# Performance work log

Hardware: AMD Instinct MI355X
Metric: run time of the kernel (lower is better)

Reference implementation:

```python
import jax, jax.numpy as jnp
import numpy as np

N_EMBED = 64
HEAD_SIZE = 64
B, T = 4096, 128

def setup_inputs() -> dict:
    key = jax.random.key(0)
    k0, k1, k2, k3 = jax.random.split(key, 4)
    x = jax.random.normal(k0, (B, T, N_EMBED), dtype=jnp.float32)
    # nn.Linear(N_EMBED, head_size, bias=False): weight shape [head_size, N_EMBED], y = x @ W.T
    Wq = jax.random.normal(k1, (HEAD_SIZE, N_EMBED), dtype=jnp.float32) * (1.0 / np.sqrt(N_EMBED))
    Wk = jax.random.normal(k2, (HEAD_SIZE, N_EMBED), dtype=jnp.float32) * (1.0 / np.sqrt(N_EMBED))
    Wv = jax.random.normal(k3, (HEAD_SIZE, N_EMBED), dtype=jnp.float32) * (1.0 / np.sqrt(N_EMBED))
    return {"x": x, "Wq": Wq, "Wk": Wk, "Wv": Wv}

def reference(x, Wq, Wk, Wv):
    # q,k,v: [B,T,H]
    q = jnp.einsum('btc,hc->bth', x, Wq)
    k = jnp.einsum('btc,hc->bth', x, Wk)
    v = jnp.einsum('btc,hc->bth', x, Wv)
    scale = HEAD_SIZE ** -0.5
    scores = jnp.einsum('bth,bsh->bts', q, k) * scale  # [B,T,T]
    Tdim = x.shape[1]
    causal = jnp.tril(jnp.ones((Tdim, Tdim), dtype=bool))
    scores = jnp.where(causal, scores, -jnp.inf)
    weights = jax.nn.softmax(scores, axis=-1)
    # dropout disabled (eval mode) for deterministic reference
    out = jnp.einsum('bts,bsh->bth', weights, v)  # [B,T,H]
    return out
```

## Files before the change

### kernel.cpp

```cpp
#include <hip/hip_runtime.h>
#include <hip/hip_bf16.h>

typedef float f4  __attribute__((ext_vector_type(4)));
typedef short s8v __attribute__((ext_vector_type(8)));
typedef short s4v __attribute__((ext_vector_type(4)));

#define MFMA16(a, b, c) __builtin_amdgcn_mfma_f32_16x16x32_bf16((a), (b), (c), 0, 0, 0)

__device__ __forceinline__ unsigned cvtpk(float a, float b) {
  __hip_bfloat162 h2 = __float22bfloat162_rn(make_float2(a, b));
  unsigned u;
  __builtin_memcpy(&u, &h2, 4);
  return u;
}
__device__ __forceinline__ s8v cvt8(const float* p) {
  float4 a = *(const float4*)p;
  float4 b = *(const float4*)(p + 4);
  union { unsigned u[4]; s8v v; } r;
  r.u[0] = cvtpk(a.x, a.y); r.u[1] = cvtpk(a.z, a.w);
  r.u[2] = cvtpk(b.x, b.y); r.u[3] = cvtpk(b.z, b.w);
  return r.v;
}
__device__ __forceinline__ s8v mk8(unsigned a0, unsigned a1, unsigned b0, unsigned b1) {
  union { unsigned u[4]; s8v v; } r;
  r.u[0] = a0; r.u[1] = a1; r.u[2] = b0; r.u[3] = b1;
  return r.v;
}
__device__ __forceinline__ s8v ld44(const short* p0, const short* p1) {
  s4v a = *(const s4v*)p0;
  s4v b = *(const s4v*)p1;
  s8v r;
  r[0] = a[0]; r[1] = a[1]; r[2] = a[2]; r[3] = a[3];
  r[4] = b[0]; r[5] = b[1]; r[6] = b[2]; r[7] = b[3];
  return r;
}

__global__ void conv_w(const void* __restrict__ wq, const void* __restrict__ wk,
                       const void* __restrict__ wv, unsigned short* __restrict__ wsp) {
  const int tid = threadIdx.x;
  const void* srcs[3] = {wq, wk, wv};
  #pragma unroll
  for (int wi = 0; wi < 3; wi++) {
    s4v* dst = (s4v*)(wsp + wi * 4096);
    const float4* s = (const float4*)srcs[wi];
    for (int i = tid; i < 1024; i += 256) {
      float4 v = s[i];
      union { unsigned u[2]; s4v v4; } p;
      p.u[0] = cvtpk(v.x, v.y); p.u[1] = cvtpk(v.z, v.w);
      dst[i] = p.v4;
    }
  }
}

__global__ __launch_bounds__(256, 4)
void attn_head(const void* __restrict__ xg, const void* __restrict__ wqp,
               const void* __restrict__ wkp, const void* __restrict__ wvp,
               void* __restrict__ outg, int xbf, int wbf) {
  __shared__ __align__(16) short smem[16384];
  short* Ksm = smem;
  short* Vt  = smem + 8192;

  const int tid  = threadIdx.x;
  const int wave = tid >> 6;
  const int lane = tid & 63;
  const int c16  = lane & 15;
  const int quad = lane >> 4;
  const int b    = blockIdx.x;
  const int swz  = c16 << 2;

  const int mts[2] = {wave, 7 - wave};

  s8v xf[2][2];
  #pragma unroll
  for (int mi = 0; mi < 2; mi++) {
    const size_t base = (size_t)b * 8192 + (size_t)(mts[mi] * 16 + c16) * 64;
    #pragma unroll
    for (int kt = 0; kt < 2; kt++) {
      const int off = kt * 32 + quad * 8;
      if (xbf) xf[mi][kt] = *(const s8v*)((const unsigned short*)xg + base + off);
      else     xf[mi][kt] = cvt8((const float*)xg + base + off);
    }
  }

  unsigned qpk[2][4][2];
  #pragma unroll
  for (int ht = 0; ht < 4; ht++) {
    s8v wqf[2], wkf[2], wvf[2];
    const int woff0 = (ht * 16 + c16) * 64 + quad * 8;
    #pragma unroll
    for (int kt = 0; kt < 2; kt++) {
      const int off = woff0 + kt * 32;
      if (wbf) {
        wqf[kt] = *(const s8v*)((const unsigned short*)wqp + off);
        wkf[kt] = *(const s8v*)((const unsigned short*)wkp + off);
        wvf[kt] = *(const s8v*)((const unsigned short*)wvp + off);
      } else {
        wqf[kt] = cvt8((const float*)wqp + off);
        wkf[kt] = cvt8((const float*)wkp + off);
        wvf[kt] = cvt8((const float*)wvp + off);
      }
    }
    #pragma unroll
    for (int mi = 0; mi < 2; mi++) {
      const int m = mts[mi];
      f4 z = {0.f, 0.f, 0.f, 0.f};
      f4 qt = z, kk = z, vv = z;
      qt = MFMA16(wqf[0], xf[mi][0], qt);  qt = MFMA16(wqf[1], xf[mi][1], qt);
      kk = MFMA16(wkf[0], xf[mi][0], kk);  kk = MFMA16(wkf[1], xf[mi][1], kk);
      vv = MFMA16(xf[mi][0], wvf[0], vv);  vv = MFMA16(xf[mi][1], wvf[1], vv);
      qpk[mi][ht][0] = cvtpk(qt[0] * 0.125f, qt[1] * 0.125f);
      qpk[mi][ht][1] = cvtpk(qt[2] * 0.125f, qt[3] * 0.125f);
      {
        union { unsigned u[2]; s4v v; } pk;
        pk.u[0] = cvtpk(kk[0], kk[1]); pk.u[1] = cvtpk(kk[2], kk[3]);
        *(s4v*)(Ksm + (m * 16 + c16) * 64 + ((ht * 16 + quad * 4) ^ swz)) = pk.v;
      }
      {
        union { unsigned u[2]; s4v v; } pv;
        pv.u[0] = cvtpk(vv[0], vv[1]); pv.u[1] = cvtpk(vv[2], vv[3]);
        *(s4v*)(Vt + (ht * 16 + c16) * 128 + ((m * 16 + quad * 4) ^ swz)) = pv.v;
      }
    }
  }

  __syncthreads();

  #pragma unroll
  for (int mi = 0; mi < 2; mi++) {
    const int m = mts[mi];
    const int q4 = quad * 4;
    const s8v qb0 = mk8(qpk[mi][0][0], qpk[mi][0][1], qpk[mi][1][0], qpk[mi][1][1]);
    const s8v qb1 = mk8(qpk[mi][2][0], qpk[mi][2][1], qpk[mi][3][0], qpk[mi][3][1]);

    f4 acc[4];
    #pragma unroll
    for (int ht = 0; ht < 4; ht++) { f4 z = {0.f,0.f,0.f,0.f}; acc[ht] = z; }
    float sumA = 0.f, sumB = 0.f;
    const int nchunk = (m >> 1) + 1;

    #pragma unroll
    for (int kt = 0; kt < 4; kt++) {
      if (kt >= nchunk) continue;
      const int nt0 = 2 * kt, nt1 = 2 * kt + 1;
      const bool hb = nt1 <= m;

      f4 z = {0.f, 0.f, 0.f, 0.f};
      f4 s0 = z, s1 = z;
      {
        const short* kr = Ksm + (nt0 * 16 + c16) * 64;
        s0 = MFMA16(ld44(kr + ((q4     ) ^ swz), kr + ((q4 + 16) ^ swz)), qb0, s0);
        s0 = MFMA16(ld44(kr + ((q4 + 32) ^ swz), kr + ((q4 + 48) ^ swz)), qb1, s0);
      }
      if (hb) {
        const short* kr = Ksm + (nt1 * 16 + c16) * 64;
        s1 = MFMA16(ld44(kr + ((q4     ) ^ swz), kr + ((q4 + 16) ^ swz)), qb0, s1);
        s1 = MFMA16(ld44(kr + ((q4 + 32) ^ swz), kr + ((q4 + 48) ^ swz)), qb1, s1);
      }
      #pragma unroll
      for (int r = 0; r < 4; r++) {
        const bool k0 = (nt0 < m) || (q4 + r <= c16);
        float e0 = k0 ? __expf(s0[r]) : 0.0f;
        s0[r] = e0; sumA += e0;
      }
      if (hb) {
        #pragma unroll
        for (int r = 0; r < 4; r++) {
          const bool k1 = (nt1 < m) || (q4 + r <= c16);
          float e1 = k1 ? __expf(s1[r]) : 0.0f;
          s1[r] = e1; sumB += e1;
        }
      }
      const s8v pb = mk8(cvtpk(s0[0], s0[1]), cvtpk(s0[2], s0[3]),
                         cvtpk(s1[0], s1[1]), cvtpk(s1[2], s1[3]));
      #pragma unroll
      for (int ht = 0; ht < 4; ht++) {
        const short* vr = Vt + (ht * 16 + c16) * 128;
        const s8v va = ld44(vr + ((kt * 32 + q4     ) ^ swz),
                            vr + ((kt * 32 + q4 + 16) ^ swz));
        acc[ht] = MFMA16(va, pb, acc[ht]);
      }
    }

    float sum = sumA + sumB;
    sum += __shfl_xor(sum, 16);
    sum += __shfl_xor(sum, 32);
    const float inv = 1.0f / sum;

    if (xbf) {
      unsigned short* op = (unsigned short*)outg + (size_t)b * 8192;
      #pragma unroll
      for (int ht = 0; ht < 4; ht++) {
        union { unsigned u[2]; s4v v; } o;
        o.u[0] = cvtpk(acc[ht][0] * inv, acc[ht][1] * inv);
        o.u[1] = cvtpk(acc[ht][2] * inv, acc[ht][3] * inv);
        *(s4v*)(op + (size_t)(m * 16 + c16) * 64 + ht * 16 + quad * 4) = o.v;
      }
    } else {
      float* op = (float*)outg + (size_t)b * 8192;
      #pragma unroll
      for (int ht = 0; ht < 4; ht++) {
        float4 o = {acc[ht][0] * inv, acc[ht][1] * inv,
                    acc[ht][2] * inv, acc[ht][3] * inv};
        *(float4*)(op + (size_t)(m * 16 + c16) * 64 + ht * 16 + quad * 4) = o;
      }
    }
  }
}

extern "C" void kernel_launch(void* const* d_in, const int* in_sizes, int n_in,
                              void* d_out, int out_size, void* d_ws, size_t ws_size,
                              hipStream_t stream) {
  (void)out_size;
  const int xbytes_bf16 = 4096 * 128 * 64 * 2;
  const int wbytes_bf16 = 64 * 64 * 2;
  const int xbf = (n_in > 0 && in_sizes[0] == xbytes_bf16) ? 1 : 0;
  const int wbf = (n_in > 1 && in_sizes[1] == wbytes_bf16) ? 1 : 0;

  if (!wbf && ws_size >= 3 * 4096 * sizeof(unsigned short)) {
    unsigned short* wsp = (unsigned short*)d_ws;
    conv_w<<<dim3(1), dim3(256), 0, stream>>>(d_in[1], d_in[2], d_in[3], wsp);
    attn_head<<<dim3(4096), dim3(256), 0, stream>>>(
        d_in[0], wsp, wsp + 4096, wsp + 8192, d_out, xbf, 1);
  } else {
    attn_head<<<dim3(4096), dim3(256), 0, stream>>>(
        d_in[0], d_in[1], d_in[2], d_in[3], d_out, xbf, wbf);
  }
}
```

Measured before the change: 273.1 us.

## Make attention blocks persistent over four batches with prefetched x loads

The grid shrinks from 4096 to 1024 blocks, and each block now loops over four batch elements. The first x tile for the next batch is prefetched into registers during the attention phase, and the second tile is loaded before the projection, so global latency overlaps compute. The projection loop is reordered to run mi outer and ht inner, so weight fragments are reloaded per mi. Launch bounds drop from 4 to 3 blocks per CU, and with only 1024 blocks on 256 CUs, occupancy and tail balance may suffer.

```diff
diff --git a/kernel.cpp b/kernel.cpp
--- a/kernel.cpp
+++ b/kernel.cpp
@@ -13,13 +13,14 @@
   __builtin_memcpy(&u, &h2, 4);
   return u;
 }
-__device__ __forceinline__ s8v cvt8(const float* p) {
-  float4 a = *(const float4*)p;
-  float4 b = *(const float4*)(p + 4);
+__device__ __forceinline__ s8v pk8(float4 a, float4 b) {
   union { unsigned u[4]; s8v v; } r;
   r.u[0] = cvtpk(a.x, a.y); r.u[1] = cvtpk(a.z, a.w);
   r.u[2] = cvtpk(b.x, b.y); r.u[3] = cvtpk(b.z, b.w);
   return r.v;
+}
+__device__ __forceinline__ s8v cvt8(const float* p) {
+  return pk8(*(const float4*)p, *(const float4*)(p + 4));
 }
 __device__ __forceinline__ s8v mk8(unsigned a0, unsigned a1, unsigned b0, unsigned b1) {
   union { unsigned u[4]; s8v v; } r;
@@ -52,7 +53,10 @@
   }
 }
 
-__global__ __launch_bounds__(256, 4)
+#define NBLK 1024
+#define NIT  4
+
+__global__ __launch_bounds__(256, 3)
 void attn_head(const void* __restrict__ xg, const void* __restrict__ wqp,
                const void* __restrict__ wkp, const void* __restrict__ wvp,
                void* __restrict__ outg, int xbf, int wbf) {
@@ -65,145 +69,196 @@
   const int lane = tid & 63;
   const int c16  = lane & 15;
   const int quad = lane >> 4;
-  const int b    = blockIdx.x;
+  const int b0   = blockIdx.x;
   const int swz  = c16 << 2;
 
   const int mts[2] = {wave, 7 - wave};
+  int xoff[2][2];
+  #pragma unroll
+  for (int mi = 0; mi < 2; mi++)
+    #pragma unroll
+    for (int kt = 0; kt < 2; kt++)
+      xoff[mi][kt] = (mts[mi] * 16 + c16) * 64 + kt * 32 + quad * 8;
 
   s8v xf[2][2];
-  #pragma unroll
-  for (int mi = 0; mi < 2; mi++) {
-    const size_t base = (size_t)b * 8192 + (size_t)(mts[mi] * 16 + c16) * 64;
+  float4 xr0[4];
+
+  if (xbf) {
+    const unsigned short* xp = (const unsigned short*)xg + (size_t)b0 * 8192;
+    xf[0][0] = *(const s8v*)(xp + xoff[0][0]);
+    xf[0][1] = *(const s8v*)(xp + xoff[0][1]);
+  } else {
+    const float* xp = (const float*)xg + (size_t)b0 * 8192;
+    xr0[0] = *(const float4*)(xp + xoff[0][0]);
+    xr0[1] = *(const float4*)(xp + xoff[0][0] + 4);
+    xr0[2] = *(const float4*)(xp + xoff[0][1]);
+    xr0[3] = *(const float4*)(xp + xoff[0][1] + 4);
+  }
+
+  for (int it = 0; it < NIT; ++it) {
+    const int b = b0 + NBLK * it;
+
+    if (!xbf) {
+      xf[0][0] = pk8(xr0[0], xr0[1]);
+      xf[0][1] = pk8(xr0[2], xr0[3]);
+    }
+    float4 xr1[4];
+    if (xbf) {
+      const unsigned short* xp = (const unsigned short*)xg + (size_t)b * 8192;
+      xf[1][0] = *(const s8v*)(xp + xoff[1][0]);
+      xf[1][1] = *(const s8v*)(xp + xoff[1][1]);
+    } else {
+      const float* xp = (const float*)xg + (size_t)b * 8192;
+      xr1[0] = *(const float4*)(xp + xoff[1][0]);
+      xr1[1] = *(const float4*)(xp + xoff[1][0] + 4);
+      xr1[2] = *(const float4*)(xp + xoff[1][1]);
+      xr1[3] = *(const float4*)(xp + xoff[1][1] + 4);
+    }
+
+    unsigned qpk[2][4][2];
     #pragma unroll
-    for (int kt = 0; kt < 2; kt++) {
-      const int off = kt * 32 + quad * 8;
-      if (xbf) xf[mi][kt] = *(const s8v*)((const unsigned short*)xg + base + off);
-      else     xf[mi][kt] = cvt8((const float*)xg + base + off);
-    }
-  }
-
-  unsigned qpk[2][4][2];
-  #pragma unroll
-  for (int ht = 0; ht < 4; ht++) {
-    s8v wqf[2], wkf[2], wvf[2];
-    const int woff0 = (ht * 16 + c16) * 64 + quad * 8;
-    #pragma unroll
-    for (int kt = 0; kt < 2; kt++) {
-      const int off = woff0 + kt * 32;
-      if (wbf) {
-        wqf[kt] = *(const s8v*)((const unsigned short*)wqp + off);
-        wkf[kt] = *(const s8v*)((const unsigned short*)wkp + off);
-        wvf[kt] = *(const s8v*)((const unsigned short*)wvp + off);
+    for (int mi = 0; mi < 2; mi++) {
+      if (mi == 1 && !xbf) {
+        xf[1][0] = pk8(xr1[0], xr1[1]);
+        xf[1][1] = pk8(xr1[2], xr1[3]);
+      }
+      const int m = mts[mi];
+      #pragma unroll
+      for (int ht = 0; ht < 4; ht++) {
+        s8v wqf[2], wkf[2], wvf[2];
+        const int woff0 = (ht * 16 + c16) * 64 + quad * 8;
+        #pragma unroll
+        for (int kt = 0; kt < 2; kt++) {
+          const int off = woff0 + kt * 32;
+          if (wbf) {
+            wqf[kt] = *(const s8v*)((const unsigned short*)wqp + off);
+            wkf[kt] = *(const s8v*)((const unsigned short*)wkp + off);
+            wvf[kt] = *(const s8v*)((const unsigned short*)wvp + off);
+          } else {
+            wqf[kt] = cvt8((const float*)wqp + off);
+            wkf[kt] = cvt8((const float*)wkp + off);
+            wvf[kt] = cvt8((const float*)wvp + off);
+          }
+        }
+        f4 z = {0.f, 0.f, 0.f, 0.f};
+        f4 qt = z, kk = z, vv = z;
+        qt = MFMA16(wqf[0], xf[mi][0], qt);  qt = MFMA16(wqf[1], xf[mi][1], qt);
+        kk = MFMA16(wkf[0], xf[mi][0], kk);  kk = MFMA16(wkf[1], xf[mi][1], kk);
+        vv = MFMA16(xf[mi][0], wvf[0], vv);  vv = MFMA16(xf[mi][1], wvf[1], vv);
+        qpk[mi][ht][0] = cvtpk(qt[0] * 0.125f, qt[1] * 0.125f);
+        qpk[mi][ht][1] = cvtpk(qt[2] * 0.125f, qt[3] * 0.125f);
+        {
+          union { unsigned u[2]; s4v v; } pk;
+          pk.u[0] = cvtpk(kk[0], kk[1]); pk.u[1] = cvtpk(kk[2], kk[3]);
+          *(s4v*)(Ksm + (m * 16 + c16) * 64 + ((ht * 16 + quad * 4) ^ swz)) = pk.v;
+        }
+        {
+          union { unsigned u[2]; s4v v; } pv;
+          pv.u[0] = cvtpk(vv[0], vv[1]); pv.u[1] = cvtpk(vv[2], vv[3]);
+          *(s4v*)(Vt + (ht * 16 + c16) * 128 + ((m * 16 + quad * 4) ^ swz)) = pv.v;
+        }
+      }
+    }
+
+    __syncthreads();
+
+    if (it + 1 < NIT) {
+      if (xbf) {
+        const unsigned short* xp = (const unsigned short*)xg +
+                                   (size_t)(b + NBLK) * 8192;
+        xf[0][0] = *(const s8v*)(xp + xoff[0][0]);
+        xf[0][1] = *(const s8v*)(xp + xoff[0][1]);
       } else {
-        wqf[kt] = cvt8((const float*)wqp + off);
-        wkf[kt] = cvt8((const float*)wkp + off);
-        wvf[kt] = cvt8((const float*)wvp + off);
-      }
-    }
+        const float* xp = (const float*)xg + (size_t)(b + NBLK) * 8192;
+        xr0[0] = *(const float4*)(xp + xoff[0][0]);
+        xr0[1] = *(const float4*)(xp + xoff[0][0] + 4);
+        xr0[2] = *(const float4*)(xp + xoff[0][1]);
+        xr0[3] = *(const float4*)(xp + xoff[0][1] + 4);
+      }
+    }
+
     #pragma unroll
     for (int mi = 0; mi < 2; mi++) {
       const int m = mts[mi];
-      f4 z = {0.f, 0.f, 0.f, 0.f};
-      f4 qt = z, kk = z, vv = z;
-      qt = MFMA16(wqf[0], xf[mi][0], qt);  qt = MFMA16(wqf[1], xf[mi][1], qt);
-      kk = MFMA16(wkf[0], xf[mi][0], kk);  kk = MFMA16(wkf[1], xf[mi][1], kk);
-      vv = MFMA16(xf[mi][0], wvf[0], vv);  vv = MFMA16(xf[mi][1], wvf[1], vv);
-      qpk[mi][ht][0] = cvtpk(qt[0] * 0.125f, qt[1] * 0.125f);
-      qpk[mi][ht][1] = cvtpk(qt[2] * 0.125f, qt[3] * 0.125f);
-      {
-        union { unsigned u[2]; s4v v; } pk;
-        pk.u[0] = cvtpk(kk[0], kk[1]); pk.u[1] = cvtpk(kk[2], kk[3]);
-        *(s4v*)(Ksm + (m * 16 + c16) * 64 + ((ht * 16 + quad * 4) ^ swz)) = pk.v;
-      }
-      {
-        union { unsigned u[2]; s4v v; } pv;
-        pv.u[0] = cvtpk(vv[0], vv[1]); pv.u[1] = cvtpk(vv[2], vv[3]);
-        *(s4v*)(Vt + (ht * 16 + c16) * 128 + ((m * 16 + quad * 4) ^ swz)) = pv.v;
-      }
-    }
-  }
-
-  __syncthreads();
-
-  #pragma unroll
-  for (int mi = 0; mi < 2; mi++) {
-    const int m = mts[mi];
-    const int q4 = quad * 4;
-    const s8v qb0 = mk8(qpk[mi][0][0], qpk[mi][0][1], qpk[mi][1][0], qpk[mi][1][1]);
-    const s8v qb1 = mk8(qpk[mi][2][0], qpk[mi][2][1], qpk[mi][3][0], qpk[mi][3][1]);
-
-    f4 acc[4];
-    #pragma unroll
-    for (int ht = 0; ht < 4; ht++) { f4 z = {0.f,0.f,0.f,0.f}; acc[ht] = z; }
-    float sumA = 0.f, sumB = 0.f;
-    const int nchunk = (m >> 1) + 1;
-
-    #pragma unroll
-    for (int kt = 0; kt < 4; kt++) {
-      if (kt >= nchunk) continue;
-      const int nt0 = 2 * kt, nt1 = 2 * kt + 1;
-      const bool hb = nt1 <= m;
-
-      f4 z = {0.f, 0.f, 0.f, 0.f};
-      f4 s0 = z, s1 = z;
-      {
-        const short* kr = Ksm + (nt0 * 16 + c16) * 64;
-        s0 = MFMA16(ld44(kr + ((q4     ) ^ swz), kr + ((q4 + 16) ^ swz)), qb0, s0);
-        s0 = MFMA16(ld44(kr + ((q4 + 32) ^ swz), kr + ((q4 + 48) ^ swz)), qb1, s0);
-      }
-      if (hb) {
-        const short* kr = Ksm + (nt1 * 16 + c16) * 64;
-        s1 = MFMA16(ld44(kr + ((q4     ) ^ swz), kr + ((q4 + 16) ^ swz)), qb0, s1);
-        s1 = MFMA16(ld44(kr + ((q4 + 32) ^ swz), kr + ((q4 + 48) ^ swz)), qb1, s1);
-      }
+      const int q4 = quad * 4;
+      const s8v qb0 = mk8(qpk[mi][0][0], qpk[mi][0][1], qpk[mi][1][0], qpk[mi][1][1]);
+      const s8v qb1 = mk8(qpk[mi][2][0], qpk[mi][2][1], qpk[mi][3][0], qpk[mi][3][1]);
+
+      f4 acc[4];
       #pragma unroll
-      for (int r = 0; r < 4; r++) {
-        const bool k0 = (nt0 < m) || (q4 + r <= c16);
-        float e0 = k0 ? __expf(s0[r]) : 0.0f;
-        s0[r] = e0; sumA += e0;
-      }
-      if (hb) {
+      for (int ht = 0; ht < 4; ht++) { f4 z = {0.f,0.f,0.f,0.f}; acc[ht] = z; }
+      float sumA = 0.f, sumB = 0.f;
+      const int nchunk = (m >> 1) + 1;
+
+      #pragma unroll
+      for (int kt = 0; kt < 4; kt++) {
+        if (kt >= nchunk) continue;
+        const int nt0 = 2 * kt, nt1 = 2 * kt + 1;
+        const bool hb = nt1 <= m;
+
+        f4 z = {0.f, 0.f, 0.f, 0.f};
+        f4 s0 = z, s1 = z;
+        {
+          const short* kr = Ksm + (nt0 * 16 + c16) * 64;
+          s0 = MFMA16(ld44(kr + ((q4     ) ^ swz), kr + ((q4 + 16) ^ swz)), qb0, s0);
+          s0 = MFMA16(ld44(kr + ((q4 + 32) ^ swz), kr + ((q4 + 48) ^ swz)), qb1, s0);
+        }
+        if (hb) {
+          const short* kr = Ksm + (nt1 * 16 + c16) * 64;
+          s1 = MFMA16(ld44(kr + ((q4     ) ^ swz), kr + ((q4 + 16) ^ swz)), qb0, s1);
+          s1 = MFMA16(ld44(kr + ((q4 + 32) ^ swz), kr + ((q4 + 48) ^ swz)), qb1, s1);
+        }
         #pragma unroll
         for (int r = 0; r < 4; r++) {
-          const bool k1 = (nt1 < m) || (q4 + r <= c16);
-          float e1 = k1 ? __expf(s1[r]) : 0.0f;
-          s1[r] = e1; sumB += e1;
-        }
-      }
-      const s8v pb = mk8(cvtpk(s0[0], s0[1]), cvtpk(s0[2], s0[3]),
-                         cvtpk(s1[0], s1[1]), cvtpk(s1[2], s1[3]));
-      #pragma unroll
-      for (int ht = 0; ht < 4; ht++) {
-        const short* vr = Vt + (ht * 16 + c16) * 128;
-        const s8v va = ld44(vr + ((kt * 32 + q4     ) ^ swz),
-                            vr + ((kt * 32 + q4 + 16) ^ swz));
-        acc[ht] = MFMA16(va, pb, acc[ht]);
-      }
-    }
-
-    float sum = sumA + sumB;
-    sum += __shfl_xor(sum, 16);
-    sum += __shfl_xor(sum, 32);
-    const float inv = 1.0f / sum;
-
-    if (xbf) {
-      unsigned short* op = (unsigned short*)outg + (size_t)b * 8192;
-      #pragma unroll
-      for (int ht = 0; ht < 4; ht++) {
-        union { unsigned u[2]; s4v v; } o;
-        o.u[0] = cvtpk(acc[ht][0] * inv, acc[ht][1] * inv);
-        o.u[1] = cvtpk(acc[ht][2] * inv, acc[ht][3] * inv);
-        *(s4v*)(op + (size_t)(m * 16 + c16) * 64 + ht * 16 + quad * 4) = o.v;
-      }
-    } else {
-      float* op = (float*)outg + (size_t)b * 8192;
-      #pragma unroll
-      for (int ht = 0; ht < 4; ht++) {
-        float4 o = {acc[ht][0] * inv, acc[ht][1] * inv,
-                    acc[ht][2] * inv, acc[ht][3] * inv};
-        *(float4*)(op + (size_t)(m * 16 + c16) * 64 + ht * 16 + quad * 4) = o;
-      }
-    }
+          const bool k0 = (nt0 < m) || (q4 + r <= c16);
+          float e0 = k0 ? __expf(s0[r]) : 0.0f;
+          s0[r] = e0; sumA += e0;
+        }
+        if (hb) {
+          #pragma unroll
+          for (int r = 0; r < 4; r++) {
+            const bool k1 = (nt1 < m) || (q4 + r <= c16);
+            float e1 = k1 ? __expf(s1[r]) : 0.0f;
+            s1[r] = e1; sumB += e1;
+          }
+        }
+        const s8v pb = mk8(cvtpk(s0[0], s0[1]), cvtpk(s0[2], s0[3]),
+                           cvtpk(s1[0], s1[1]), cvtpk(s1[2], s1[3]));
+        #pragma unroll
+        for (int ht = 0; ht < 4; ht++) {
+          const short* vr = Vt + (ht * 16 + c16) * 128;
+          const s8v va = ld44(vr + ((kt * 32 + q4     ) ^ swz),
+                              vr + ((kt * 32 + q4 + 16) ^ swz));
+          acc[ht] = MFMA16(va, pb, acc[ht]);
+        }
+      }
+
+      float sum = sumA + sumB;
+      sum += __shfl_xor(sum, 16);
+      sum += __shfl_xor(sum, 32);
+      const float inv = 1.0f / sum;
+
+      if (xbf) {
+        unsigned short* op = (unsigned short*)outg + (size_t)b * 8192;
+        #pragma unroll
+        for (int ht = 0; ht < 4; ht++) {
+          union { unsigned u[2]; s4v v; } o;
+          o.u[0] = cvtpk(acc[ht][0] * inv, acc[ht][1] * inv);
+          o.u[1] = cvtpk(acc[ht][2] * inv, acc[ht][3] * inv);
+          *(s4v*)(op + (size_t)(m * 16 + c16) * 64 + ht * 16 + q4) = o.v;
+        }
+      } else {
+        float* op = (float*)outg + (size_t)b * 8192;
+        #pragma unroll
+        for (int ht = 0; ht < 4; ht++) {
+          float4 o = {acc[ht][0] * inv, acc[ht][1] * inv,
+                      acc[ht][2] * inv, acc[ht][3] * inv};
+          *(float4*)(op + (size_t)(m * 16 + c16) * 64 + ht * 16 + q4) = o;
+        }
+      }
+    }
+
+    if (it + 1 < NIT) __syncthreads();
   }
 }
 
@@ -219,10 +274,10 @@
   if (!wbf && ws_size >= 3 * 4096 * sizeof(unsigned short)) {
     unsigned short* wsp = (unsigned short*)d_ws;
     conv_w<<<dim3(1), dim3(256), 0, stream>>>(d_in[1], d_in[2], d_in[3], wsp);
-    attn_head<<<dim3(4096), dim3(256), 0, stream>>>(
+    attn_head<<<dim3(NBLK), dim3(256), 0, stream>>>(
         d_in[0], wsp, wsp + 4096, wsp + 8192, d_out, xbf, 1);
   } else {
-    attn_head<<<dim3(4096), dim3(256), 0, stream>>>(
+    attn_head<<<dim3(NBLK), dim3(256), 0, stream>>>(
         d_in[0], d_in[1], d_in[2], d_in[3], d_out, xbf, wbf);
   }
 }
```

Result: slower. 412.8 us (+51.2%).
